# Kernel tuning notes

Measured on AMD Instinct MI355X. Metric: run time of the kernel, lower is better.

Reference implementation:

```python
import jax, jax.numpy as jnp
import numpy as np

FRAMES, RANK = 128, 5          # rank=5 implied by create_adj6 non_adj index lists (max index 4)
N = FRAMES * RANK              # 640 nodes
B, NFEAT, NHID, NCLASS = 128, 256, 8, 16
ALPHA = 0.2                    # LeakyReLU negative slope
MASK_VAL = -9e15               # hard mask value from the torch code


def create_adj6(frames, rank):
    """Block-diagonal (with holes) + chain adjacency, exactly as in the torch source."""
    adj = np.zeros((frames * rank, frames * rank), dtype=np.float32)
    non_adj_x = [0, 0, 1, 2, 3, 3, 4, 4]
    non_adj_y = [3, 4, 4, 3, 0, 2, 0, 1]
    for i in range(frames):
        adj[rank * i:rank * (i + 1), rank * i:rank * (i + 1)] = 1
        for j in range(len(non_adj_x)):
            adj[rank * i + non_adj_x[j], rank * i + non_adj_y[j]] = 0
        for j in range(rank):
            if i > 0:
                adj[rank * i + j, rank * (i - 1) + j] = 1
            if i < frames - 1:
                adj[rank * i + j, rank * (i + 1) + j] = 1
    return adj


def _xavier(key, shape):
    fan_in, fan_out = shape[0], shape[1]
    std = np.sqrt(2.0) * np.sqrt(2.0 / (fan_in + fan_out))  # gain=sqrt(2) xavier_normal
    return std * jax.random.normal(key, shape, dtype=jnp.float32)


def setup_inputs() -> dict:
    key = jax.random.key(0)
    ks = jax.random.split(key, 7)
    x = jax.random.normal(ks[0], (B, N, NFEAT), dtype=jnp.float32)
    W1 = _xavier(ks[1], (NFEAT, NHID))
    a11 = _xavier(ks[2], (NHID, 1))
    a12 = _xavier(ks[3], (NHID, 1))
    W2 = _xavier(ks[4], (NHID, NCLASS))  # nhid*nheads=8 -> nclass=16
    a21 = _xavier(ks[5], (NCLASS, 1))
    a22 = _xavier(ks[6], (NCLASS, 1))
    adj = jnp.asarray(create_adj6(FRAMES, RANK) > 0)  # bool [N, N]
    return dict(x=x, W1=W1, a11=a11, a12=a12, W2=W2, a21=a21, a22=a22, adj=adj)


def gat_layer(xi, adj, W, a1, a2):
    # xi: [N, F_in]
    h = xi @ W                              # [N, F_out]
    f1 = h @ a1                             # [N, 1]
    f2 = h @ a2                             # [N, 1]
    e = jax.nn.leaky_relu(f1 + f2.T, negative_slope=ALPHA)  # [N, N]
    scores = jnp.where(adj, e, jnp.float32(MASK_VAL))        # hard additive-style mask
    att = jax.nn.softmax(scores, axis=-1)   # dropout disabled (eval mode)
    return att @ h                          # [N, F_out]


def reference(x, W1, a11, a12, W2, a21, a22, adj):
    def single(xi):
        h1 = gat_layer(xi, adj, W1, a11, a12)          # concat=False -> no elu inside layer
        h2 = jax.nn.elu(gat_layer(h1, adj, W2, a21, a22))
        return jax.nn.log_softmax(h2, axis=1)          # [N, NCLASS]
    return jax.vmap(single)(x)                          # [B, N, NCLASS]
```

## Files before the change

kernel.cpp:

```cpp
#include <hip/hip_runtime.h>
#include <stdint.h>

#define B_ 128
#define N_ 640
#define NFEAT 256
#define NHID 8
#define NCLASS 16
#define RANK 5
#define FRAMES 128
#define ALPHA 0.2f
#define PACKMASK 30236135u

typedef short bf16x8 __attribute__((ext_vector_type(8)));
typedef float f32x4  __attribute__((ext_vector_type(4)));
typedef unsigned int u32x4 __attribute__((ext_vector_type(4)));

#define GA_ROWS 64
#define GA_GRID (B_ * N_ / GA_ROWS)

__device__ __forceinline__ void cvt8(float4 p, float4 q, bf16x8& hi, bf16x8& lo)
{
    float v[8] = {p.x, p.y, p.z, p.w, q.x, q.y, q.z, q.w};
    u32x4 hw, lw;
#pragma unroll
    for (int i = 0; i < 4; ++i) {
        const unsigned ua = __float_as_uint(v[2 * i]);
        const unsigned ub = __float_as_uint(v[2 * i + 1]);
        hw[i] = (ua >> 16) | (ub & 0xFFFF0000u);
        const float la = v[2 * i]     - __uint_as_float(ua & 0xFFFF0000u);
        const float lb = v[2 * i + 1] - __uint_as_float(ub & 0xFFFF0000u);
        const unsigned va = __float_as_uint(la), vb = __float_as_uint(lb);
        lw[i] = ((va + 0x7FFFu + ((va >> 16) & 1u)) >> 16)
              | ((vb + 0x7FFFu + ((vb >> 16) & 1u)) & 0xFFFF0000u);
    }
    hi = __builtin_bit_cast(bf16x8, hw);
    lo = __builtin_bit_cast(bf16x8, lw);
}

__global__ void __launch_bounds__(256, 4) k_gemm(
    const float* __restrict__ x, const float* __restrict__ W1,
    float* __restrict__ h1ws)
{
    __shared__ float xs[2][GA_ROWS * 32];
    const int tid = threadIdx.x;
    const int w   = tid >> 6;
    const int l   = tid & 63;
    const int rowbase = blockIdx.x * GA_ROWS;

    const int n  = l & 15;
    const int kg = (l >> 4) << 3;
    bf16x8 bhi[8], blo[8];
#pragma unroll
    for (int ks = 0; ks < 8; ++ks) {
        u32x4 hw, lw;
#pragma unroll
        for (int p = 0; p < 4; ++p) {
            float wa = 0.0f, wb = 0.0f;
            if (n < NHID) {
                const int k0 = ks * 32 + kg + 2 * p;
                wa = W1[k0 * NHID + n];
                wb = W1[(k0 + 1) * NHID + n];
            }
            const unsigned ua = __float_as_uint(wa), ub = __float_as_uint(wb);
            hw[p] = (ua >> 16) | (ub & 0xFFFF0000u);
            const float la = wa - __uint_as_float(ua & 0xFFFF0000u);
            const float lb = wb - __uint_as_float(ub & 0xFFFF0000u);
            const unsigned va = __float_as_uint(la), vb = __float_as_uint(lb);
            lw[p] = ((va + 0x7FFFu + ((va >> 16) & 1u)) >> 16)
                  | ((vb + 0x7FFFu + ((vb >> 16) & 1u)) & 0xFFFF0000u);
        }
        bhi[ks] = __builtin_bit_cast(bf16x8, hw);
        blo[ks] = __builtin_bit_cast(bf16x8, lw);
    }

    auto stage = [&](int ks, int buf) {
#pragma unroll
        for (int rr = 0; rr < 2; ++rr) {
            const int r  = rr * 32 + (tid >> 3);
            const int fo = (tid & 7) * 4;
            const int ff = fo ^ ((r & 3) << 3);
            const float* gsrc = x + (size_t)(rowbase + r) * NFEAT + ks * 32 + ff;
            const float* lbase = &xs[buf][rr * 1024 + w * 256];
            __builtin_amdgcn_global_load_lds(
                (const __attribute__((address_space(1))) unsigned int*)(const void*)gsrc,
                (__attribute__((address_space(3))) unsigned int*)(void*)lbase,
                16, 0, 0);
        }
    };

    const int Rrow = w * 16 + (l & 15);
    const int gsw  = kg ^ ((Rrow & 3) << 3);
    const int aoff = Rrow * 32 + gsw;

    f32x4 acc = {0.f, 0.f, 0.f, 0.f};
    stage(0, 0);
    __syncthreads();

#pragma unroll
    for (int ks = 0; ks < 8; ++ks) {
        const int cur = ks & 1;
        if (ks < 7) stage(ks + 1, cur ^ 1);
        const float* ap = &xs[cur][aoff];
        const float4 p = *reinterpret_cast<const float4*>(ap);
        const float4 q = *reinterpret_cast<const float4*>(ap + 4);
        bf16x8 ahi, alo;
        cvt8(p, q, ahi, alo);
        acc = __builtin_amdgcn_mfma_f32_16x16x32_bf16(ahi, bhi[ks], acc, 0, 0, 0);
        acc = __builtin_amdgcn_mfma_f32_16x16x32_bf16(alo, bhi[ks], acc, 0, 0, 0);
        acc = __builtin_amdgcn_mfma_f32_16x16x32_bf16(ahi, blo[ks], acc, 0, 0, 0);
        __syncthreads();
    }

    if (n < NHID) {
        float* hp = h1ws + ((size_t)rowbase + w * 16 + (l >> 4) * 4) * NHID + n;
#pragma unroll
        for (int j = 0; j < 4; ++j) hp[j * NHID] = acc[j];
    }
}

#define QSPLIT 8
#define TFRAMES (FRAMES / QSPLIT)
#define TCOUNT (TFRAMES * RANK)
#define BLOCKB 128
#define MAXSTAGE 100
#define H1S 9
#define H2S 17

#define OFF_F1S (MAXSTAGE * H1S)
#define OFF_F2S (OFF_F1S + MAXSTAGE)
#define OFF_G1S (MAXSTAGE * H2S)
#define OFF_G2S (OFF_G1S + MAXSTAGE)
#define SMEMF (OFF_G2S + MAXSTAGE)

__device__ __forceinline__ float lrelu(float v) { return v >= 0.0f ? v : ALPHA * v; }

__global__ void __launch_bounds__(BLOCKB, 8) k_attn(
    const float* __restrict__ h1ws,
    const float* __restrict__ a11, const float* __restrict__ a12,
    const float* __restrict__ W2, const float* __restrict__ a21, const float* __restrict__ a22,
    float* __restrict__ out)
{
    __shared__ float smem[SMEMF];
    float* h1s = smem;
    float* f1s = smem + OFF_F1S;
    float* f2s = smem + OFF_F2S;
    float* h2s = smem;
    float* g1s = smem + OFF_G1S;
    float* g2s = smem + OFF_G2S;

    const int bid = blockIdx.x;
    const int bq  = (bid & 7) * 128 + (bid >> 3);
    const int b   = bq >> 3;
    const int q   = bq & 7;

    const int tf_lo  = q * TFRAMES;
    const int l1f_lo = max(tf_lo - 1, 0);
    const int l1f_hi = min(tf_lo + TFRAMES, FRAMES - 1);
    const int stf_lo = max(tf_lo - 2, 0);
    const int stf_hi = min(tf_lo + TFRAMES + 1, FRAMES - 1);
    const int stage_lo  = stf_lo * RANK;
    const int stage_cnt = (stf_hi - stf_lo + 1) * RANK;
    const int l1_lo  = l1f_lo * RANK;
    const int l1_cnt = (l1f_hi - l1f_lo + 1) * RANK;
    const int t_lo   = tf_lo * RANK;

    const int tid = threadIdx.x;

    if (tid < stage_cnt) {
        const float* hp = h1ws + ((size_t)b * N_ + stage_lo + tid) * NHID;
        const float4 p = *reinterpret_cast<const float4*>(hp);
        const float4 q4 = *reinterpret_cast<const float4*>(hp + 4);
        float hv[NHID] = {p.x, p.y, p.z, p.w, q4.x, q4.y, q4.z, q4.w};
        float s1 = 0.0f, s2 = 0.0f;
#pragma unroll
        for (int k = 0; k < NHID; ++k) {
            s1 = fmaf(hv[k], a11[k], s1);
            s2 = fmaf(hv[k], a12[k], s2);
            h1s[tid * H1S + k] = hv[k];
        }
        f1s[tid] = s1;
        f2s[tid] = s2;
    }
    __syncthreads();

    float h2[NCLASS];
    float s1g = 0.0f, s2g = 0.0f;
    const bool actL1 = (tid < l1_cnt);
    if (actL1) {
        const int u  = l1_lo + tid;
        const int fr = u / RANK;
        const int ru = u - fr * RANK;
        const unsigned rm = (PACKMASK >> (5 * ru)) & 31u;
        const int loc      = u - stage_lo;
        const int base_loc = fr * RANK - stage_lo;
        const bool hp = (fr > 0), hn = (fr < FRAMES - 1);
        const float fu = f1s[loc];

        float m = -1e30f;
        if (hp) m = fmaxf(m, lrelu(fu + f2s[loc - RANK]));
#pragma unroll
        for (int rv = 0; rv < RANK; ++rv)
            if (rm & (1u << rv)) m = fmaxf(m, lrelu(fu + f2s[base_loc + rv]));
        if (hn) m = fmaxf(m, lrelu(fu + f2s[loc + RANK]));

        float s = 0.0f;
        float o1[NHID];
#pragma unroll
        for (int k = 0; k < NHID; ++k) o1[k] = 0.0f;

        auto acc1 = [&](int vloc) {
            float w = __expf(lrelu(fu + f2s[vloc]) - m);
            s += w;
#pragma unroll
            for (int k = 0; k < NHID; ++k) o1[k] = fmaf(w, h1s[vloc * H1S + k], o1[k]);
        };
        if (hp) acc1(loc - RANK);
#pragma unroll
        for (int rv = 0; rv < RANK; ++rv)
            if (rm & (1u << rv)) acc1(base_loc + rv);
        if (hn) acc1(loc + RANK);

        const float inv = 1.0f / s;
#pragma unroll
        for (int k = 0; k < NHID; ++k) o1[k] *= inv;

#pragma unroll
        for (int c = 0; c < NCLASS; ++c) {
            float t = 0.0f;
#pragma unroll
            for (int k = 0; k < NHID; ++k) t = fmaf(o1[k], W2[k * NCLASS + c], t);
            h2[c] = t;
            s1g = fmaf(t, a21[c], s1g);
            s2g = fmaf(t, a22[c], s2g);
        }
    }
    __syncthreads();

    if (actL1) {
        const int loc = l1_lo + tid - stage_lo;
#pragma unroll
        for (int c = 0; c < NCLASS; ++c) h2s[loc * H2S + c] = h2[c];
        g1s[loc] = s1g;
        g2s[loc] = s2g;
    }
    __syncthreads();

    if (tid < TCOUNT) {
        const int u  = t_lo + tid;
        const int fr = u / RANK;
        const int ru = u - fr * RANK;
        const unsigned rm = (PACKMASK >> (5 * ru)) & 31u;
        const int loc      = u - stage_lo;
        const int base_loc = fr * RANK - stage_lo;
        const bool hp = (fr > 0), hn = (fr < FRAMES - 1);
        const float gu = g1s[loc];

        float m = -1e30f;
        if (hp) m = fmaxf(m, lrelu(gu + g2s[loc - RANK]));
#pragma unroll
        for (int rv = 0; rv < RANK; ++rv)
            if (rm & (1u << rv)) m = fmaxf(m, lrelu(gu + g2s[base_loc + rv]));
        if (hn) m = fmaxf(m, lrelu(gu + g2s[loc + RANK]));

        float s = 0.0f;
        float o2[NCLASS];
#pragma unroll
        for (int c = 0; c < NCLASS; ++c) o2[c] = 0.0f;

        auto acc2 = [&](int vloc) {
            float w = __expf(lrelu(gu + g2s[vloc]) - m);
            s += w;
#pragma unroll
            for (int c = 0; c < NCLASS; ++c) o2[c] = fmaf(w, h2s[vloc * H2S + c], o2[c]);
        };
        if (hp) acc2(loc - RANK);
#pragma unroll
        for (int rv = 0; rv < RANK; ++rv)
            if (rm & (1u << rv)) acc2(base_loc + rv);
        if (hn) acc2(loc + RANK);

        const float inv = 1.0f / s;
#pragma unroll
        for (int c = 0; c < NCLASS; ++c) o2[c] *= inv;

#pragma unroll
        for (int c = 0; c < NCLASS; ++c) o2[c] = (o2[c] > 0.0f) ? o2[c] : __expf(o2[c]) - 1.0f;

        float mm = o2[0];
#pragma unroll
        for (int c = 1; c < NCLASS; ++c) mm = fmaxf(mm, o2[c]);
        float ss = 0.0f;
#pragma unroll
        for (int c = 0; c < NCLASS; ++c) ss += __expf(o2[c] - mm);
        const float ls = mm + __logf(ss);

        float* op = out + ((size_t)b * N_ + u) * NCLASS;
#pragma unroll
        for (int c = 0; c < NCLASS; c += 4)
            *reinterpret_cast<float4*>(op + c) =
                make_float4(o2[c] - ls, o2[c + 1] - ls, o2[c + 2] - ls, o2[c + 3] - ls);
    }
}

extern "C" void kernel_launch(void* const* d_in, const int* in_sizes, int n_in,
                              void* d_out, int out_size, void* d_ws, size_t ws_size,
                              hipStream_t stream)
{
    const float* x   = (const float*)d_in[0];
    const float* W1  = (const float*)d_in[1];
    const float* a11 = (const float*)d_in[2];
    const float* a12 = (const float*)d_in[3];
    const float* W2  = (const float*)d_in[4];
    const float* a21 = (const float*)d_in[5];
    const float* a22 = (const float*)d_in[6];
    float* outp  = (float*)d_out;
    float* h1ws  = (float*)d_ws;

    k_gemm<<<GA_GRID, 256, 0, stream>>>(x, W1, h1ws);
    k_attn<<<B_ * QSPLIT, BLOCKB, 0, stream>>>(h1ws, a11, a12, W2, a21, a22, outp);
}
```

Baseline: 28.77 us.

## Load GEMM inputs directly to registers and split attention into finer tiles

```diff
diff --git a/kernel.cpp b/kernel.cpp
--- a/kernel.cpp
+++ b/kernel.cpp
@@ -37,11 +37,10 @@
     lo = __builtin_bit_cast(bf16x8, lw);
 }
 
-__global__ void __launch_bounds__(256, 4) k_gemm(
+__global__ void __launch_bounds__(256) k_gemm(
     const float* __restrict__ x, const float* __restrict__ W1,
     float* __restrict__ h1ws)
 {
-    __shared__ float xs[2][GA_ROWS * 32];
     const int tid = threadIdx.x;
     const int w   = tid >> 6;
     const int l   = tid & 63;
@@ -49,6 +48,15 @@
 
     const int n  = l & 15;
     const int kg = (l >> 4) << 3;
+
+    const float* xrow = x + (size_t)(rowbase + w * 16 + n) * NFEAT + kg;
+    float4 xv[16];
+#pragma unroll
+    for (int ks = 0; ks < 8; ++ks) {
+        xv[2 * ks]     = *reinterpret_cast<const float4*>(xrow + ks * 32);
+        xv[2 * ks + 1] = *reinterpret_cast<const float4*>(xrow + ks * 32 + 4);
+    }
+
     bf16x8 bhi[8], blo[8];
 #pragma unroll
     for (int ks = 0; ks < 8; ++ks) {
@@ -73,42 +81,14 @@
         blo[ks] = __builtin_bit_cast(bf16x8, lw);
     }
 
-    auto stage = [&](int ks, int buf) {
-#pragma unroll
-        for (int rr = 0; rr < 2; ++rr) {
-            const int r  = rr * 32 + (tid >> 3);
-            const int fo = (tid & 7) * 4;
-            const int ff = fo ^ ((r & 3) << 3);
-            const float* gsrc = x + (size_t)(rowbase + r) * NFEAT + ks * 32 + ff;
-            const float* lbase = &xs[buf][rr * 1024 + w * 256];
-            __builtin_amdgcn_global_load_lds(
-                (const __attribute__((address_space(1))) unsigned int*)(const void*)gsrc,
-                (__attribute__((address_space(3))) unsigned int*)(void*)lbase,
-                16, 0, 0);
-        }
-    };
-
-    const int Rrow = w * 16 + (l & 15);
-    const int gsw  = kg ^ ((Rrow & 3) << 3);
-    const int aoff = Rrow * 32 + gsw;
-
     f32x4 acc = {0.f, 0.f, 0.f, 0.f};
-    stage(0, 0);
-    __syncthreads();
-
 #pragma unroll
     for (int ks = 0; ks < 8; ++ks) {
-        const int cur = ks & 1;
-        if (ks < 7) stage(ks + 1, cur ^ 1);
-        const float* ap = &xs[cur][aoff];
-        const float4 p = *reinterpret_cast<const float4*>(ap);
-        const float4 q = *reinterpret_cast<const float4*>(ap + 4);
         bf16x8 ahi, alo;
-        cvt8(p, q, ahi, alo);
+        cvt8(xv[2 * ks], xv[2 * ks + 1], ahi, alo);
         acc = __builtin_amdgcn_mfma_f32_16x16x32_bf16(ahi, bhi[ks], acc, 0, 0, 0);
         acc = __builtin_amdgcn_mfma_f32_16x16x32_bf16(alo, bhi[ks], acc, 0, 0, 0);
         acc = __builtin_amdgcn_mfma_f32_16x16x32_bf16(ahi, blo[ks], acc, 0, 0, 0);
-        __syncthreads();
     }
 
     if (n < NHID) {
@@ -118,11 +98,11 @@
     }
 }
 
-#define QSPLIT 8
+#define QSPLIT 16
 #define TFRAMES (FRAMES / QSPLIT)
 #define TCOUNT (TFRAMES * RANK)
-#define BLOCKB 128
-#define MAXSTAGE 100
+#define BLOCKB 64
+#define MAXSTAGE 60
 #define H1S 9
 #define H2S 17
 
@@ -149,9 +129,9 @@
     float* g2s = smem + OFF_G2S;
 
     const int bid = blockIdx.x;
-    const int bq  = (bid & 7) * 128 + (bid >> 3);
-    const int b   = bq >> 3;
-    const int q   = bq & 7;
+    const int bq  = (bid & 7) * 256 + (bid >> 3);
+    const int b   = bq >> 4;
+    const int q   = bq & 15;
 
     const int tf_lo  = q * TFRAMES;
     const int l1f_lo = max(tf_lo - 1, 0);
```

After: 32.58 us. +13.2%, slower.
